# Optimization experiments

Hardware: AMD Instinct MI355X
Metric: run time of the kernel (lower is better)

## Reference

```python
import jax, jax.numpy as jnp
import numpy as np

B, T = 512, 2048
IN1, H1, H2 = 1, 64, 16


def _lstm_params(key, in_dim, hid):
    k = 1.0 / np.sqrt(hid)
    ks = jax.random.split(key, 4)
    u = lambda kk, shape: jax.random.uniform(kk, shape, jnp.float32, -k, k)
    return (u(ks[0], (4 * hid, in_dim)),  # w_ih, PyTorch gate order i,f,g,o
            u(ks[1], (4 * hid, hid)),     # w_hh
            u(ks[2], (4 * hid,)),         # b_ih
            u(ks[3], (4 * hid,)))         # b_hh


def setup_inputs() -> dict:
    key = jax.random.key(0)
    kx, k1, k2 = jax.random.split(key, 3)
    x = jax.random.normal(kx, (B, T, IN1), dtype=jnp.float32)
    w_ih1, w_hh1, b_ih1, b_hh1 = _lstm_params(k1, IN1, H1)
    w_ih2, w_hh2, b_ih2, b_hh2 = _lstm_params(k2, H1, H2)
    return {"x": x,
            "w_ih1": w_ih1, "w_hh1": w_hh1, "b_ih1": b_ih1, "b_hh1": b_hh1,
            "w_ih2": w_ih2, "w_hh2": w_hh2, "b_ih2": b_ih2, "b_hh2": b_hh2}


def _lstm(x, w_ih, w_hh, b_ih, b_hh):
    # x: [B, T, in]; returns all hidden states [B, T, H]
    hid = w_hh.shape[1]
    # precompute input contribution for every timestep: [T, B, 4H]
    xg = jnp.einsum('bti,gi->tbg', x, w_ih) + b_ih + b_hh
    h0 = jnp.zeros((x.shape[0], hid), x.dtype)
    c0 = jnp.zeros((x.shape[0], hid), x.dtype)

    def step(carry, xt):
        h, c = carry
        gates = xt + h @ w_hh.T                       # [B, 4H]
        i, f, g, o = jnp.split(gates, 4, axis=-1)     # PyTorch order
        i = jax.nn.sigmoid(i)
        f = jax.nn.sigmoid(f)
        g = jnp.tanh(g)
        o = jax.nn.sigmoid(o)
        c = f * c + i * g
        h = o * jnp.tanh(c)
        return (h, c), h

    _, hs = jax.lax.scan(step, (h0, c0), xg)          # hs: [T, B, H]
    return jnp.transpose(hs, (1, 0, 2))               # [B, T, H]


def reference(x, w_ih1, w_hh1, b_ih1, b_hh1, w_ih2, w_hh2, b_ih2, b_hh2):
    h1 = _lstm(x, w_ih1, w_hh1, b_ih1, b_hh1)   # [B, T, 64]
    h2 = _lstm(h1, w_ih2, w_hh2, b_ih2, b_hh2)  # [B, T, 16]
    return h2
```

## Files before the change

kernel.cpp:

```cpp
#include <hip/hip_runtime.h>

#define TSTEPS 2048
#define NBATCH 512
#define H1 64
#define H2 16

typedef _Float16 h2v __attribute__((ext_vector_type(2)));

__device__ __forceinline__ float fsig(float x) {
    return __builtin_amdgcn_rcpf(1.0f + __builtin_amdgcn_exp2f(-1.4426950408889634f * x));
}
__device__ __forceinline__ float ftanh(float x) {
    return 1.0f - 2.0f * __builtin_amdgcn_rcpf(1.0f + __builtin_amdgcn_exp2f(2.8853900817779268f * x));
}
__device__ __forceinline__ float act(float x, float k2) {
    return k2 * fsig(k2 * x) - (k2 - 1.0f);
}

#if __has_builtin(__builtin_amdgcn_fdot2)
__device__ __forceinline__ float dot2(int wp, int hp, float acc) {
    return __builtin_amdgcn_fdot2(__builtin_bit_cast(h2v, wp),
                                  __builtin_bit_cast(h2v, hp), acc, false);
}
#else
__device__ __forceinline__ float dot2(int wp, int hp, float acc) {
    h2v a = __builtin_bit_cast(h2v, wp), b = __builtin_bit_cast(h2v, hp);
    return acc + (float)a.x * (float)b.x + (float)a.y * (float)b.y;
}
#endif

__device__ __forceinline__ int packh2(float a, float b) {
    h2v v; v.x = (_Float16)a; v.y = (_Float16)b;
    return __builtin_bit_cast(int, v);
}
template<int CTRL>
__device__ __forceinline__ float dpp_bcast(float v) {
    int r = __builtin_amdgcn_mov_dpp(__float_as_int(v), CTRL, 0xF, 0xF, true);
    return __int_as_float(r);
}

__global__ void __launch_bounds__(64, 1)
__attribute__((amdgpu_waves_per_eu(1, 1)))
lstm2_fused(const float* __restrict__ x,
            const float* __restrict__ w_ih1,
            const float* __restrict__ w_hh1,
            const float* __restrict__ b_ih1,
            const float* __restrict__ b_hh1,
            const float* __restrict__ w_ih2,
            const float* __restrict__ w_hh2,
            const float* __restrict__ b_ih2,
            const float* __restrict__ b_hh2,
            float* __restrict__ out)
{
    const int lane = threadIdx.x;
    const int b    = blockIdx.x;

    __shared__ int4     wlds[26][64];
    __shared__ float    x_lds[TSTEPS];
    __shared__ _Float16 h1_lds[H1];
    __shared__ _Float16 h2_lds[H2];
    __shared__ float    ring[32][H2];

    {
        const float4* xs = (const float4*)(x + (size_t)b * TSTEPS);
        float4* xd = (float4*)x_lds;
        #pragma unroll
        for (int i = 0; i < 8; ++i) xd[lane + 64 * i] = xs[lane + 64 * i];
    }
    if (lane < 32) ((int*)h1_lds)[lane] = 0;
    if (lane < 8)  ((int*)h2_lds)[lane] = 0;

    int w1i[32], w1f[32];
    {
        const float* wri = w_hh1 + (size_t)lane * H1;
        const float* wrf = w_hh1 + (size_t)(H1 + lane) * H1;
        #pragma unroll
        for (int k = 0; k < 32; ++k) {
            w1i[k] = packh2(wri[2 * k], wri[2 * k + 1]);
            w1f[k] = packh2(wrf[2 * k], wrf[2 * k + 1]);
        }
    }
    const int m  = lane >> 2;
    const int g2 = lane & 3;
    const int r2 = g2 * H2 + m;
    {
        const float* wrg = w_hh1 + (size_t)(2 * H1 + lane) * H1;
        const float* wro = w_hh1 + (size_t)(3 * H1 + lane) * H1;
        const float* wr2 = w_ih2 + (size_t)r2 * H1;
        #pragma unroll
        for (int tq = 0; tq < 8; ++tq) {
            wlds[tq][lane] = make_int4(
                packh2(wrg[8*tq+0], wrg[8*tq+1]), packh2(wrg[8*tq+2], wrg[8*tq+3]),
                packh2(wrg[8*tq+4], wrg[8*tq+5]), packh2(wrg[8*tq+6], wrg[8*tq+7]));
            wlds[8 + tq][lane] = make_int4(
                packh2(wro[8*tq+0], wro[8*tq+1]), packh2(wro[8*tq+2], wro[8*tq+3]),
                packh2(wro[8*tq+4], wro[8*tq+5]), packh2(wro[8*tq+6], wro[8*tq+7]));
            wlds[16 + tq][lane] = make_int4(
                packh2(wr2[8*tq+0], wr2[8*tq+1]), packh2(wr2[8*tq+2], wr2[8*tq+3]),
                packh2(wr2[8*tq+4], wr2[8*tq+5]), packh2(wr2[8*tq+6], wr2[8*tq+7]));
        }
        const float* wrh = w_hh2 + (size_t)r2 * H2;
        wlds[24][lane] = make_int4(packh2(wrh[0], wrh[1]),  packh2(wrh[2], wrh[3]),
                                   packh2(wrh[4], wrh[5]),  packh2(wrh[6], wrh[7]));
        wlds[25][lane] = make_int4(packh2(wrh[8], wrh[9]),  packh2(wrh[10], wrh[11]),
                                   packh2(wrh[12], wrh[13]), packh2(wrh[14], wrh[15]));
    }

    const float wxi = w_ih1[lane],        wxf = w_ih1[H1 + lane];
    const float wxg = w_ih1[2*H1 + lane], wxo = w_ih1[3*H1 + lane];
    const float bsi = b_ih1[lane] + b_hh1[lane];
    const float bsf = b_ih1[H1+lane] + b_hh1[H1+lane];
    const float bsg = b_ih1[2*H1+lane] + b_hh1[2*H1+lane];
    const float bso = b_ih1[3*H1+lane] + b_hh1[3*H1+lane];
    const float bs2 = b_ih2[r2] + b_hh2[r2];
    const float k22 = (g2 == 2) ? 2.0f : 1.0f;

    float c1 = 0.0f;
    float c2 = 0.0f;
    float* outb = out + (size_t)b * TSTEPS * H2;

    const int4* wl = &wlds[0][0];

    for (int p = 0; p <= TSTEPS; ++p) {
        const int tau_f = p - 1;
        if (tau_f >= 31 && (tau_f & 15) == 15) {
            const int tau0 = (tau_f & ~15) - 16;
            const int tt = tau0 + (lane >> 2), ch0 = (lane & 3) * 4;
            float4 v = *(const float4*)&ring[tt & 31][ch0];
            *(float4*)(outb + (size_t)tt * H2 + ch0) = v;
        }

        const float xv = x_lds[p & (TSTEPS - 1)];
        float ai = bsi + wxi * xv;
        float af = bsf + wxf * xv;
        float ag = bsg + wxg * xv;
        float ao = bso + wxo * xv;
        float a0 = bs2, a1 = 0.f, a2a = 0.f, a3 = 0.f;
        int4 vh0, vh1;

        {
            const int4* hs4 = (const int4*)h1_lds;
            #pragma unroll
            for (int c = 0; c < 4; ++c) {
                int4 hA = hs4[2*c], hB = hs4[2*c + 1];
                int4 cg  = wl[(2*c)      * 64 + lane];
                int4 cg2 = wl[(2*c + 1)  * 64 + lane];
                int4 co  = wl[(8 + 2*c)  * 64 + lane];
                int4 co2 = wl[(9 + 2*c)  * 64 + lane];
                int4 cu  = wl[(16 + 2*c) * 64 + lane];
                int4 cu2 = wl[(17 + 2*c) * 64 + lane];
                if (c == 2) { vh0 = wl[24 * 64 + lane]; vh1 = wl[25 * 64 + lane]; }

                ai = dot2(w1i[8*c+0], hA.x, ai); ai = dot2(w1i[8*c+1], hA.y, ai);
                ai = dot2(w1i[8*c+2], hA.z, ai); ai = dot2(w1i[8*c+3], hA.w, ai);
                ai = dot2(w1i[8*c+4], hB.x, ai); ai = dot2(w1i[8*c+5], hB.y, ai);
                ai = dot2(w1i[8*c+6], hB.z, ai); ai = dot2(w1i[8*c+7], hB.w, ai);

                af = dot2(w1f[8*c+0], hA.x, af); af = dot2(w1f[8*c+1], hA.y, af);
                af = dot2(w1f[8*c+2], hA.z, af); af = dot2(w1f[8*c+3], hA.w, af);
                af = dot2(w1f[8*c+4], hB.x, af); af = dot2(w1f[8*c+5], hB.y, af);
                af = dot2(w1f[8*c+6], hB.z, af); af = dot2(w1f[8*c+7], hB.w, af);

                ag = dot2(cg.x,  hA.x, ag); ag = dot2(cg.y,  hA.y, ag);
                ag = dot2(cg.z,  hA.z, ag); ag = dot2(cg.w,  hA.w, ag);
                ag = dot2(cg2.x, hB.x, ag); ag = dot2(cg2.y, hB.y, ag);
                ag = dot2(cg2.z, hB.z, ag); ag = dot2(cg2.w, hB.w, ag);

                ao = dot2(co.x,  hA.x, ao); ao = dot2(co.y,  hA.y, ao);
                ao = dot2(co.z,  hA.z, ao); ao = dot2(co.w,  hA.w, ao);
                ao = dot2(co2.x, hB.x, ao); ao = dot2(co2.y, hB.y, ao);
                ao = dot2(co2.z, hB.z, ao); ao = dot2(co2.w, hB.w, ao);

                a0  = dot2(cu.x,  hA.x, a0);  a1  = dot2(cu.y,  hA.y, a1);
                a2a = dot2(cu.z,  hA.z, a2a); a3  = dot2(cu.w,  hA.w, a3);
                a0  = dot2(cu2.x, hB.x, a0);  a1  = dot2(cu2.y, hB.y, a1);
                a2a = dot2(cu2.z, hB.z, a2a); a3  = dot2(cu2.w, hB.w, a3);
            }
        }

        if (p < TSTEPS) {
            float gi = fsig(ai), gf = fsig(af), gg = ftanh(ag), go = fsig(ao);
            c1 = gf * c1 + gi * gg;
            float h1n = go * ftanh(c1);
            h1_lds[lane] = (_Float16)h1n;
        }

        if (p >= 1) {
            const int4* hs = (const int4*)h2_lds;
            int4 u0 = hs[0], u1 = hs[1];
            a0  = dot2(vh0.x, u0.x, a0);  a1  = dot2(vh0.y, u0.y, a1);
            a2a = dot2(vh0.z, u0.z, a2a); a3  = dot2(vh0.w, u0.w, a3);
            a0  = dot2(vh1.x, u1.x, a0);  a1  = dot2(vh1.y, u1.y, a1);
            a2a = dot2(vh1.z, u1.z, a2a); a3  = dot2(vh1.w, u1.w, a3);
            float av = act((a0 + a1) + (a2a + a3), k22);
            float gi = dpp_bcast<0x00>(av);
            float gf = dpp_bcast<0x55>(av);
            float gg = dpp_bcast<0xAA>(av);
            float go = dpp_bcast<0xFF>(av);
            c2 = gf * c2 + gi * gg;
            float h2n = go * ftanh(c2);
            if (g2 == 0) {
                h2_lds[m] = (_Float16)h2n;
                ring[(p - 1) & 31][m] = h2n;
            }
        }
    }

    {
        const int tt = 2032 + (lane >> 2), ch0 = (lane & 3) * 4;
        float4 v = *(const float4*)&ring[tt & 31][ch0];
        *(float4*)(outb + (size_t)tt * H2 + ch0) = v;
    }
}

extern "C" void kernel_launch(void* const* d_in, const int* in_sizes, int n_in,
                              void* d_out, int out_size, void* d_ws, size_t ws_size,
                              hipStream_t stream) {
    const float* x     = (const float*)d_in[0];
    const float* w_ih1 = (const float*)d_in[1];
    const float* w_hh1 = (const float*)d_in[2];
    const float* b_ih1 = (const float*)d_in[3];
    const float* b_hh1 = (const float*)d_in[4];
    const float* w_ih2 = (const float*)d_in[5];
    const float* w_hh2 = (const float*)d_in[6];
    const float* b_ih2 = (const float*)d_in[7];
    const float* b_hh2 = (const float*)d_in[8];
    float* out = (float*)d_out;

    lstm2_fused<<<NBATCH, 64, 0, stream>>>(x, w_ih1, w_hh1, b_ih1, b_hh1,
                                           w_ih2, w_hh2, b_ih2, b_hh2, out);
}
```

Baseline: 1.170 ms.

## Broadcast hidden states via readlane/DPP into SGPRs instead of LDS round-trip

Replaces the per-step LDS write/read of the layer-1 and layer-2 hidden vectors with cross-lane communication: each lane packs its fp16 hidden value with its neighbour's via a DPP xor-1 swap, and v_readlane broadcasts the packed pairs into uniform registers that feed the dot products directly. It also splits each gate accumulator into two partial sums to shorten the serial dependency chain. This removes LDS store-to-load latency and waitcnt stalls from the recurrent critical path, at the cost of 40 readlane instructions per step, which are serialising VALU-to-SGPR moves, plus added register pressure.

```diff
diff --git a/kernel.cpp b/kernel.cpp
--- a/kernel.cpp
+++ b/kernel.cpp
@@ -37,6 +37,9 @@
 __device__ __forceinline__ float dpp_bcast(float v) {
     int r = __builtin_amdgcn_mov_dpp(__float_as_int(v), CTRL, 0xF, 0xF, true);
     return __int_as_float(r);
+}
+__device__ __forceinline__ int dpp_xor1_i(int v) {
+    return __builtin_amdgcn_mov_dpp(v, 0xB1, 0xF, 0xF, true);
 }
 
 __global__ void __launch_bounds__(64, 1)
@@ -55,11 +58,9 @@
     const int lane = threadIdx.x;
     const int b    = blockIdx.x;
 
-    __shared__ int4     wlds[26][64];
-    __shared__ float    x_lds[TSTEPS];
-    __shared__ _Float16 h1_lds[H1];
-    __shared__ _Float16 h2_lds[H2];
-    __shared__ float    ring[32][H2];
+    __shared__ int4  wlds[26][64];
+    __shared__ float x_lds[TSTEPS];
+    __shared__ float ring[32][H2];
 
     {
         const float4* xs = (const float4*)(x + (size_t)b * TSTEPS);
@@ -67,8 +68,6 @@
         #pragma unroll
         for (int i = 0; i < 8; ++i) xd[lane + 64 * i] = xs[lane + 64 * i];
     }
-    if (lane < 32) ((int*)h1_lds)[lane] = 0;
-    if (lane < 8)  ((int*)h2_lds)[lane] = 0;
 
     int w1i[32], w1f[32];
     {
@@ -121,6 +120,13 @@
 
     const int4* wl = &wlds[0][0];
 
+    int sh[32];
+    int s2h[8];
+    #pragma unroll
+    for (int i = 0; i < 32; ++i) sh[i] = 0;
+    #pragma unroll
+    for (int i = 0; i < 8; ++i)  s2h[i] = 0;
+
     for (int p = 0; p <= TSTEPS; ++p) {
         const int tau_f = p - 1;
         if (tau_f >= 31 && (tau_f & 15) == 15) {
@@ -131,67 +137,72 @@
         }
 
         const float xv = x_lds[p & (TSTEPS - 1)];
-        float ai = bsi + wxi * xv;
-        float af = bsf + wxf * xv;
-        float ag = bsg + wxg * xv;
-        float ao = bso + wxo * xv;
+        float aiA = bsi + wxi * xv, aiB = 0.f;
+        float afA = bsf + wxf * xv, afB = 0.f;
+        float agA = bsg + wxg * xv, agB = 0.f;
+        float aoA = bso + wxo * xv, aoB = 0.f;
         float a0 = bs2, a1 = 0.f, a2a = 0.f, a3 = 0.f;
         int4 vh0, vh1;
 
-        {
-            const int4* hs4 = (const int4*)h1_lds;
-            #pragma unroll
-            for (int c = 0; c < 4; ++c) {
-                int4 hA = hs4[2*c], hB = hs4[2*c + 1];
-                int4 cg  = wl[(2*c)      * 64 + lane];
-                int4 cg2 = wl[(2*c + 1)  * 64 + lane];
-                int4 co  = wl[(8 + 2*c)  * 64 + lane];
-                int4 co2 = wl[(9 + 2*c)  * 64 + lane];
-                int4 cu  = wl[(16 + 2*c) * 64 + lane];
-                int4 cu2 = wl[(17 + 2*c) * 64 + lane];
-                if (c == 2) { vh0 = wl[24 * 64 + lane]; vh1 = wl[25 * 64 + lane]; }
-
-                ai = dot2(w1i[8*c+0], hA.x, ai); ai = dot2(w1i[8*c+1], hA.y, ai);
-                ai = dot2(w1i[8*c+2], hA.z, ai); ai = dot2(w1i[8*c+3], hA.w, ai);
-                ai = dot2(w1i[8*c+4], hB.x, ai); ai = dot2(w1i[8*c+5], hB.y, ai);
-                ai = dot2(w1i[8*c+6], hB.z, ai); ai = dot2(w1i[8*c+7], hB.w, ai);
-
-                af = dot2(w1f[8*c+0], hA.x, af); af = dot2(w1f[8*c+1], hA.y, af);
-                af = dot2(w1f[8*c+2], hA.z, af); af = dot2(w1f[8*c+3], hA.w, af);
-                af = dot2(w1f[8*c+4], hB.x, af); af = dot2(w1f[8*c+5], hB.y, af);
-                af = dot2(w1f[8*c+6], hB.z, af); af = dot2(w1f[8*c+7], hB.w, af);
-
-                ag = dot2(cg.x,  hA.x, ag); ag = dot2(cg.y,  hA.y, ag);
-                ag = dot2(cg.z,  hA.z, ag); ag = dot2(cg.w,  hA.w, ag);
-                ag = dot2(cg2.x, hB.x, ag); ag = dot2(cg2.y, hB.y, ag);
-                ag = dot2(cg2.z, hB.z, ag); ag = dot2(cg2.w, hB.w, ag);
-
-                ao = dot2(co.x,  hA.x, ao); ao = dot2(co.y,  hA.y, ao);
-                ao = dot2(co.z,  hA.z, ao); ao = dot2(co.w,  hA.w, ao);
-                ao = dot2(co2.x, hB.x, ao); ao = dot2(co2.y, hB.y, ao);
-                ao = dot2(co2.z, hB.z, ao); ao = dot2(co2.w, hB.w, ao);
-
-                a0  = dot2(cu.x,  hA.x, a0);  a1  = dot2(cu.y,  hA.y, a1);
-                a2a = dot2(cu.z,  hA.z, a2a); a3  = dot2(cu.w,  hA.w, a3);
-                a0  = dot2(cu2.x, hB.x, a0);  a1  = dot2(cu2.y, hB.y, a1);
-                a2a = dot2(cu2.z, hB.z, a2a); a3  = dot2(cu2.w, hB.w, a3);
-            }
+        #pragma unroll
+        for (int c = 0; c < 4; ++c) {
+            int4 cg  = wl[(2*c)      * 64 + lane];
+            int4 cg2 = wl[(2*c + 1)  * 64 + lane];
+            int4 co  = wl[(8 + 2*c)  * 64 + lane];
+            int4 co2 = wl[(9 + 2*c)  * 64 + lane];
+            int4 cu  = wl[(16 + 2*c) * 64 + lane];
+            int4 cu2 = wl[(17 + 2*c) * 64 + lane];
+            if (c == 2) { vh0 = wl[24 * 64 + lane]; vh1 = wl[25 * 64 + lane]; }
+            float* pi = (c < 2) ? &aiA : &aiB;
+            float* pf = (c < 2) ? &afA : &afB;
+            float* pg = (c < 2) ? &agA : &agB;
+            float* po = (c < 2) ? &aoA : &aoB;
+
+            *pi = dot2(w1i[8*c+0], sh[8*c+0], *pi); *pi = dot2(w1i[8*c+1], sh[8*c+1], *pi);
+            *pi = dot2(w1i[8*c+2], sh[8*c+2], *pi); *pi = dot2(w1i[8*c+3], sh[8*c+3], *pi);
+            *pi = dot2(w1i[8*c+4], sh[8*c+4], *pi); *pi = dot2(w1i[8*c+5], sh[8*c+5], *pi);
+            *pi = dot2(w1i[8*c+6], sh[8*c+6], *pi); *pi = dot2(w1i[8*c+7], sh[8*c+7], *pi);
+
+            *pf = dot2(w1f[8*c+0], sh[8*c+0], *pf); *pf = dot2(w1f[8*c+1], sh[8*c+1], *pf);
+            *pf = dot2(w1f[8*c+2], sh[8*c+2], *pf); *pf = dot2(w1f[8*c+3], sh[8*c+3], *pf);
+            *pf = dot2(w1f[8*c+4], sh[8*c+4], *pf); *pf = dot2(w1f[8*c+5], sh[8*c+5], *pf);
+            *pf = dot2(w1f[8*c+6], sh[8*c+6], *pf); *pf = dot2(w1f[8*c+7], sh[8*c+7], *pf);
+
+            *pg = dot2(cg.x,  sh[8*c+0], *pg); *pg = dot2(cg.y,  sh[8*c+1], *pg);
+            *pg = dot2(cg.z,  sh[8*c+2], *pg); *pg = dot2(cg.w,  sh[8*c+3], *pg);
+            *pg = dot2(cg2.x, sh[8*c+4], *pg); *pg = dot2(cg2.y, sh[8*c+5], *pg);
+            *pg = dot2(cg2.z, sh[8*c+6], *pg); *pg = dot2(cg2.w, sh[8*c+7], *pg);
+
+            *po = dot2(co.x,  sh[8*c+0], *po); *po = dot2(co.y,  sh[8*c+1], *po);
+            *po = dot2(co.z,  sh[8*c+2], *po); *po = dot2(co.w,  sh[8*c+3], *po);
+            *po = dot2(co2.x, sh[8*c+4], *po); *po = dot2(co2.y, sh[8*c+5], *po);
+            *po = dot2(co2.z, sh[8*c+6], *po); *po = dot2(co2.w, sh[8*c+7], *po);
+
+            a0  = dot2(cu.x,  sh[8*c+0], a0);  a1  = dot2(cu.y,  sh[8*c+1], a1);
+            a2a = dot2(cu.z,  sh[8*c+2], a2a); a3  = dot2(cu.w,  sh[8*c+3], a3);
+            a0  = dot2(cu2.x, sh[8*c+4], a0);  a1  = dot2(cu2.y, sh[8*c+5], a1);
+            a2a = dot2(cu2.z, sh[8*c+6], a2a); a3  = dot2(cu2.w, sh[8*c+7], a3);
         }
 
         if (p < TSTEPS) {
-            float gi = fsig(ai), gf = fsig(af), gg = ftanh(ag), go = fsig(ao);
+            float gi = fsig(aiA + aiB), gf = fsig(afA + afB);
+            float gg = ftanh(agA + agB), go = fsig(aoA + aoB);
             c1 = gf * c1 + gi * gg;
             float h1n = go * ftanh(c1);
-            h1_lds[lane] = (_Float16)h1n;
+            h2v hv; hv.x = (_Float16)h1n; hv.y = (_Float16)0.0f;
+            int h1u = __builtin_bit_cast(int, hv) & 0xFFFF;
+            int nb  = dpp_xor1_i(h1u);
+            int packed = h1u | (nb << 16);
+            #pragma unroll
+            for (int i = 0; i < 32; ++i)
+                sh[i] = __builtin_amdgcn_readlane(packed, 2 * i);
         }
 
         if (p >= 1) {
-            const int4* hs = (const int4*)h2_lds;
-            int4 u0 = hs[0], u1 = hs[1];
-            a0  = dot2(vh0.x, u0.x, a0);  a1  = dot2(vh0.y, u0.y, a1);
-            a2a = dot2(vh0.z, u0.z, a2a); a3  = dot2(vh0.w, u0.w, a3);
-            a0  = dot2(vh1.x, u1.x, a0);  a1  = dot2(vh1.y, u1.y, a1);
-            a2a = dot2(vh1.z, u1.z, a2a); a3  = dot2(vh1.w, u1.w, a3);
+            a0  = dot2(vh0.x, s2h[0], a0);  a1  = dot2(vh0.y, s2h[1], a1);
+            a2a = dot2(vh0.z, s2h[2], a2a); a3  = dot2(vh0.w, s2h[3], a3);
+            a0  = dot2(vh1.x, s2h[4], a0);  a1  = dot2(vh1.y, s2h[5], a1);
+            a2a = dot2(vh1.z, s2h[6], a2a); a3  = dot2(vh1.w, s2h[7], a3);
             float av = act((a0 + a1) + (a2a + a3), k22);
             float gi = dpp_bcast<0x00>(av);
             float gf = dpp_bcast<0x55>(av);
@@ -199,10 +210,15 @@
             float go = dpp_bcast<0xFF>(av);
             c2 = gf * c2 + gi * gg;
             float h2n = go * ftanh(c2);
-            if (g2 == 0) {
-                h2_lds[m] = (_Float16)h2n;
-                ring[(p - 1) & 31][m] = h2n;
+            h2v h2p; h2p.x = (_Float16)h2n; h2p.y = (_Float16)0.0f;
+            int h2u = __builtin_bit_cast(int, h2p) & 0xFFFF;
+            #pragma unroll
+            for (int k = 0; k < 8; ++k) {
+                int lo = __builtin_amdgcn_readlane(h2u, 8 * k);
+                int hi = __builtin_amdgcn_readlane(h2u, 8 * k + 4);
+                s2h[k] = lo | (hi << 16);
             }
+            if (g2 == 0) ring[(p - 1) & 31][m] = h2n;
         }
     }
 
```

Result: slower. 1.299 ms (+11.0%).

## Process two batch rows per wavefront to interleave independent recurrences

Applied to the files above, without the earlier changes.

Each 64-lane block now runs two batch sequences at once, so each weight load from LDS or registers is reused for two independent dot-product chains. The forget-gate weights move from registers to LDS to make room for the doubled accumulators and states. The intent is to hide the serial latency of the per-step recurrence with a second independent chain and to reuse weight loads across two rows. The grid halves to 256 blocks, so fewer wavefronts run across the CUs, and each step now does twice the work.

```diff
diff --git a/kernel.cpp b/kernel.cpp
--- a/kernel.cpp
+++ b/kernel.cpp
@@ -53,56 +53,58 @@
             float* __restrict__ out)
 {
     const int lane = threadIdx.x;
-    const int b    = blockIdx.x;
-
-    __shared__ int4     wlds[26][64];
-    __shared__ float    x_lds[TSTEPS];
-    __shared__ _Float16 h1_lds[H1];
-    __shared__ _Float16 h2_lds[H2];
-    __shared__ float    ring[32][H2];
-
-    {
-        const float4* xs = (const float4*)(x + (size_t)b * TSTEPS);
-        float4* xd = (float4*)x_lds;
+    const int b0   = blockIdx.x * 2;
+
+    __shared__ int4     wlds[34][64];
+    __shared__ float    x_lds[2][TSTEPS];
+    __shared__ _Float16 h1_lds[2][H1];
+    __shared__ _Float16 h2_lds[2][H2];
+    __shared__ float    ring[32][2][H2];
+
+    #pragma unroll
+    for (int bb = 0; bb < 2; ++bb) {
+        const float4* xs = (const float4*)(x + (size_t)(b0 + bb) * TSTEPS);
+        float4* xd = (float4*)x_lds[bb];
         #pragma unroll
         for (int i = 0; i < 8; ++i) xd[lane + 64 * i] = xs[lane + 64 * i];
     }
-    if (lane < 32) ((int*)h1_lds)[lane] = 0;
-    if (lane < 8)  ((int*)h2_lds)[lane] = 0;
-
-    int w1i[32], w1f[32];
+    h1_lds[0][lane] = (_Float16)0.0f;
+    h1_lds[1][lane] = (_Float16)0.0f;
+    if (lane < 16) { h2_lds[0][lane] = (_Float16)0.0f; h2_lds[1][lane] = (_Float16)0.0f; }
+
+    int w1i[32];
     {
         const float* wri = w_hh1 + (size_t)lane * H1;
-        const float* wrf = w_hh1 + (size_t)(H1 + lane) * H1;
-        #pragma unroll
-        for (int k = 0; k < 32; ++k) {
-            w1i[k] = packh2(wri[2 * k], wri[2 * k + 1]);
-            w1f[k] = packh2(wrf[2 * k], wrf[2 * k + 1]);
-        }
+        #pragma unroll
+        for (int k = 0; k < 32; ++k) w1i[k] = packh2(wri[2 * k], wri[2 * k + 1]);
     }
     const int m  = lane >> 2;
     const int g2 = lane & 3;
     const int r2 = g2 * H2 + m;
     {
+        const float* wrf = w_hh1 + (size_t)(H1 + lane) * H1;
         const float* wrg = w_hh1 + (size_t)(2 * H1 + lane) * H1;
         const float* wro = w_hh1 + (size_t)(3 * H1 + lane) * H1;
         const float* wr2 = w_ih2 + (size_t)r2 * H1;
         #pragma unroll
-        for (int tq = 0; tq < 8; ++tq) {
-            wlds[tq][lane] = make_int4(
-                packh2(wrg[8*tq+0], wrg[8*tq+1]), packh2(wrg[8*tq+2], wrg[8*tq+3]),
-                packh2(wrg[8*tq+4], wrg[8*tq+5]), packh2(wrg[8*tq+6], wrg[8*tq+7]));
-            wlds[8 + tq][lane] = make_int4(
-                packh2(wro[8*tq+0], wro[8*tq+1]), packh2(wro[8*tq+2], wro[8*tq+3]),
-                packh2(wro[8*tq+4], wro[8*tq+5]), packh2(wro[8*tq+6], wro[8*tq+7]));
-            wlds[16 + tq][lane] = make_int4(
-                packh2(wr2[8*tq+0], wr2[8*tq+1]), packh2(wr2[8*tq+2], wr2[8*tq+3]),
-                packh2(wr2[8*tq+4], wr2[8*tq+5]), packh2(wr2[8*tq+6], wr2[8*tq+7]));
+        for (int r = 0; r < 8; ++r) {
+            wlds[r][lane] = make_int4(
+                packh2(wrf[8*r+0], wrf[8*r+1]), packh2(wrf[8*r+2], wrf[8*r+3]),
+                packh2(wrf[8*r+4], wrf[8*r+5]), packh2(wrf[8*r+6], wrf[8*r+7]));
+            wlds[8 + r][lane] = make_int4(
+                packh2(wrg[8*r+0], wrg[8*r+1]), packh2(wrg[8*r+2], wrg[8*r+3]),
+                packh2(wrg[8*r+4], wrg[8*r+5]), packh2(wrg[8*r+6], wrg[8*r+7]));
+            wlds[16 + r][lane] = make_int4(
+                packh2(wro[8*r+0], wro[8*r+1]), packh2(wro[8*r+2], wro[8*r+3]),
+                packh2(wro[8*r+4], wro[8*r+5]), packh2(wro[8*r+6], wro[8*r+7]));
+            wlds[24 + r][lane] = make_int4(
+                packh2(wr2[8*r+0], wr2[8*r+1]), packh2(wr2[8*r+2], wr2[8*r+3]),
+                packh2(wr2[8*r+4], wr2[8*r+5]), packh2(wr2[8*r+6], wr2[8*r+7]));
         }
         const float* wrh = w_hh2 + (size_t)r2 * H2;
-        wlds[24][lane] = make_int4(packh2(wrh[0], wrh[1]),  packh2(wrh[2], wrh[3]),
+        wlds[32][lane] = make_int4(packh2(wrh[0], wrh[1]),  packh2(wrh[2], wrh[3]),
                                    packh2(wrh[4], wrh[5]),  packh2(wrh[6], wrh[7]));
-        wlds[25][lane] = make_int4(packh2(wrh[8], wrh[9]),  packh2(wrh[10], wrh[11]),
+        wlds[33][lane] = make_int4(packh2(wrh[8], wrh[9]),  packh2(wrh[10], wrh[11]),
                                    packh2(wrh[12], wrh[13]), packh2(wrh[14], wrh[15]));
     }
 
@@ -115,101 +117,128 @@
     const float bs2 = b_ih2[r2] + b_hh2[r2];
     const float k22 = (g2 == 2) ? 2.0f : 1.0f;
 
-    float c1 = 0.0f;
-    float c2 = 0.0f;
-    float* outb = out + (size_t)b * TSTEPS * H2;
+    float c1_0 = 0.f, c1_1 = 0.f;
+    float c2_0 = 0.f, c2_1 = 0.f;
+    float* outb0 = out + (size_t)b0 * TSTEPS * H2;
+    float* outb1 = out + (size_t)(b0 + 1) * TSTEPS * H2;
 
     const int4* wl = &wlds[0][0];
+
+#define DOTS1(C, hA, hB, ai, af, ag, ao, q0, q1, q2, q3) do {                  \
+    ai = dot2(w1i[8*C+0], hA.x, ai); ai = dot2(w1i[8*C+1], hA.y, ai);          \
+    ai = dot2(w1i[8*C+2], hA.z, ai); ai = dot2(w1i[8*C+3], hA.w, ai);          \
+    ai = dot2(w1i[8*C+4], hB.x, ai); ai = dot2(w1i[8*C+5], hB.y, ai);          \
+    ai = dot2(w1i[8*C+6], hB.z, ai); ai = dot2(w1i[8*C+7], hB.w, ai);          \
+    af = dot2(cf.x,  hA.x, af); af = dot2(cf.y,  hA.y, af);                    \
+    af = dot2(cf.z,  hA.z, af); af = dot2(cf.w,  hA.w, af);                    \
+    af = dot2(cf2.x, hB.x, af); af = dot2(cf2.y, hB.y, af);                    \
+    af = dot2(cf2.z, hB.z, af); af = dot2(cf2.w, hB.w, af);                    \
+    ag = dot2(cg.x,  hA.x, ag); ag = dot2(cg.y,  hA.y, ag);                    \
+    ag = dot2(cg.z,  hA.z, ag); ag = dot2(cg.w,  hA.w, ag);                    \
+    ag = dot2(cg2.x, hB.x, ag); ag = dot2(cg2.y, hB.y, ag);                    \
+    ag = dot2(cg2.z, hB.z, ag); ag = dot2(cg2.w, hB.w, ag);                    \
+    ao = dot2(co.x,  hA.x, ao); ao = dot2(co.y,  hA.y, ao);                    \
+    ao = dot2(co.z,  hA.z, ao); ao = dot2(co.w,  hA.w, ao);                    \
+    ao = dot2(co2.x, hB.x, ao); ao = dot2(co2.y, hB.y, ao);                    \
+    ao = dot2(co2.z, hB.z, ao); ao = dot2(co2.w, hB.w, ao);                    \
+    q0 = dot2(cu.x,  hA.x, q0); q1 = dot2(cu.y,  hA.y, q1);                    \
+    q2 = dot2(cu.z,  hA.z, q2); q3 = dot2(cu.w,  hA.w, q3);                    \
+    q0 = dot2(cu2.x, hB.x, q0); q1 = dot2(cu2.y, hB.y, q1);                    \
+    q2 = dot2(cu2.z, hB.z, q2); q3 = dot2(cu2.w, hB.w, q3);                    \
+} while (0)
 
     for (int p = 0; p <= TSTEPS; ++p) {
         const int tau_f = p - 1;
         if (tau_f >= 31 && (tau_f & 15) == 15) {
             const int tau0 = (tau_f & ~15) - 16;
             const int tt = tau0 + (lane >> 2), ch0 = (lane & 3) * 4;
-            float4 v = *(const float4*)&ring[tt & 31][ch0];
-            *(float4*)(outb + (size_t)tt * H2 + ch0) = v;
-        }
-
-        const float xv = x_lds[p & (TSTEPS - 1)];
-        float ai = bsi + wxi * xv;
-        float af = bsf + wxf * xv;
-        float ag = bsg + wxg * xv;
-        float ao = bso + wxo * xv;
-        float a0 = bs2, a1 = 0.f, a2a = 0.f, a3 = 0.f;
+            float4 v0 = *(const float4*)&ring[tt & 31][0][ch0];
+            float4 v1 = *(const float4*)&ring[tt & 31][1][ch0];
+            *(float4*)(outb0 + (size_t)tt * H2 + ch0) = v0;
+            *(float4*)(outb1 + (size_t)tt * H2 + ch0) = v1;
+        }
+
+        const int pm = p & (TSTEPS - 1);
+        const float xv0 = x_lds[0][pm], xv1 = x_lds[1][pm];
+        float ai0 = bsi + wxi * xv0, af0 = bsf + wxf * xv0;
+        float ag0 = bsg + wxg * xv0, ao0 = bso + wxo * xv0;
+        float ai1 = bsi + wxi * xv1, af1 = bsf + wxf * xv1;
+        float ag1 = bsg + wxg * xv1, ao1 = bso + wxo * xv1;
+        float q00 = bs2, q10 = 0.f, q20 = 0.f, q30 = 0.f;
+        float q01 = bs2, q11 = 0.f, q21 = 0.f, q31 = 0.f;
         int4 vh0, vh1;
 
-        {
-            const int4* hs4 = (const int4*)h1_lds;
-            #pragma unroll
-            for (int c = 0; c < 4; ++c) {
-                int4 hA = hs4[2*c], hB = hs4[2*c + 1];
-                int4 cg  = wl[(2*c)      * 64 + lane];
-                int4 cg2 = wl[(2*c + 1)  * 64 + lane];
-                int4 co  = wl[(8 + 2*c)  * 64 + lane];
-                int4 co2 = wl[(9 + 2*c)  * 64 + lane];
-                int4 cu  = wl[(16 + 2*c) * 64 + lane];
-                int4 cu2 = wl[(17 + 2*c) * 64 + lane];
-                if (c == 2) { vh0 = wl[24 * 64 + lane]; vh1 = wl[25 * 64 + lane]; }
-
-                ai = dot2(w1i[8*c+0], hA.x, ai); ai = dot2(w1i[8*c+1], hA.y, ai);
-                ai = dot2(w1i[8*c+2], hA.z, ai); ai = dot2(w1i[8*c+3], hA.w, ai);
-                ai = dot2(w1i[8*c+4], hB.x, ai); ai = dot2(w1i[8*c+5], hB.y, ai);
-                ai = dot2(w1i[8*c+6], hB.z, ai); ai = dot2(w1i[8*c+7], hB.w, ai);
-
-                af = dot2(w1f[8*c+0], hA.x, af); af = dot2(w1f[8*c+1], hA.y, af);
-                af = dot2(w1f[8*c+2], hA.z, af); af = dot2(w1f[8*c+3], hA.w, af);
-                af = dot2(w1f[8*c+4], hB.x, af); af = dot2(w1f[8*c+5], hB.y, af);
-                af = dot2(w1f[8*c+6], hB.z, af); af = dot2(w1f[8*c+7], hB.w, af);
-
-                ag = dot2(cg.x,  hA.x, ag); ag = dot2(cg.y,  hA.y, ag);
-                ag = dot2(cg.z,  hA.z, ag); ag = dot2(cg.w,  hA.w, ag);
-                ag = dot2(cg2.x, hB.x, ag); ag = dot2(cg2.y, hB.y, ag);
-                ag = dot2(cg2.z, hB.z, ag); ag = dot2(cg2.w, hB.w, ag);
-
-                ao = dot2(co.x,  hA.x, ao); ao = dot2(co.y,  hA.y, ao);
-                ao = dot2(co.z,  hA.z, ao); ao = dot2(co.w,  hA.w, ao);
-                ao = dot2(co2.x, hB.x, ao); ao = dot2(co2.y, hB.y, ao);
-                ao = dot2(co2.z, hB.z, ao); ao = dot2(co2.w, hB.w, ao);
-
-                a0  = dot2(cu.x,  hA.x, a0);  a1  = dot2(cu.y,  hA.y, a1);
-                a2a = dot2(cu.z,  hA.z, a2a); a3  = dot2(cu.w,  hA.w, a3);
-                a0  = dot2(cu2.x, hB.x, a0);  a1  = dot2(cu2.y, hB.y, a1);
-                a2a = dot2(cu2.z, hB.z, a2a); a3  = dot2(cu2.w, hB.w, a3);
+        const int4* hs0 = (const int4*)h1_lds[0];
+        const int4* hs1 = (const int4*)h1_lds[1];
+
+        #pragma unroll
+        for (int c = 0; c < 4; ++c) {
+            int4 cf  = wl[(2*c)      * 64 + lane];
+            int4 cf2 = wl[(2*c + 1)  * 64 + lane];
+            int4 cg  = wl[(8 + 2*c)  * 64 + lane];
+            int4 cg2 = wl[(9 + 2*c)  * 64 + lane];
+            int4 co  = wl[(16 + 2*c) * 64 + lane];
+            int4 co2 = wl[(17 + 2*c) * 64 + lane];
+            int4 cu  = wl[(24 + 2*c) * 64 + lane];
+            int4 cu2 = wl[(25 + 2*c) * 64 + lane];
+            if (c == 2) { vh0 = wl[32 * 64 + lane]; vh1 = wl[33 * 64 + lane]; }
+            int4 hA0 = hs0[2*c], hB0 = hs0[2*c + 1];
+            int4 hA1 = hs1[2*c], hB1 = hs1[2*c + 1];
+            DOTS1(c, hA0, hB0, ai0, af0, ag0, ao0, q00, q10, q20, q30);
+            DOTS1(c, hA1, hB1, ai1, af1, ag1, ao1, q01, q11, q21, q31);
+        }
+
+        if (p < TSTEPS) {
+            float gi0 = fsig(ai0), gf0 = fsig(af0), gg0 = ftanh(ag0), go0 = fsig(ao0);
+            float gi1 = fsig(ai1), gf1 = fsig(af1), gg1 = ftanh(ag1), go1 = fsig(ao1);
+            c1_0 = gf0 * c1_0 + gi0 * gg0;
+            c1_1 = gf1 * c1_1 + gi1 * gg1;
+            float h1n0 = go0 * ftanh(c1_0);
+            float h1n1 = go1 * ftanh(c1_1);
+            h1_lds[0][lane] = (_Float16)h1n0;
+            h1_lds[1][lane] = (_Float16)h1n1;
+        }
+
+        if (p >= 1) {
+            const int4* h2p0 = (const int4*)h2_lds[0];
+            const int4* h2p1 = (const int4*)h2_lds[1];
+            int4 u00 = h2p0[0], u01 = h2p0[1];
+            int4 u10 = h2p1[0], u11 = h2p1[1];
+            q00 = dot2(vh0.x, u00.x, q00); q10 = dot2(vh0.y, u00.y, q10);
+            q20 = dot2(vh0.z, u00.z, q20); q30 = dot2(vh0.w, u00.w, q30);
+            q00 = dot2(vh1.x, u01.x, q00); q10 = dot2(vh1.y, u01.y, q10);
+            q20 = dot2(vh1.z, u01.z, q20); q30 = dot2(vh1.w, u01.w, q30);
+            q01 = dot2(vh0.x, u10.x, q01); q11 = dot2(vh0.y, u10.y, q11);
+            q21 = dot2(vh0.z, u10.z, q21); q31 = dot2(vh0.w, u10.w, q31);
+            q01 = dot2(vh1.x, u11.x, q01); q11 = dot2(vh1.y, u11.y, q11);
+            q21 = dot2(vh1.z, u11.z, q21); q31 = dot2(vh1.w, u11.w, q31);
+
+            float av0 = act((q00 + q10) + (q20 + q30), k22);
+            float av1 = act((q01 + q11) + (q21 + q31), k22);
+            float gi0 = dpp_bcast<0x00>(av0), gf0 = dpp_bcast<0x55>(av0);
+            float gg0 = dpp_bcast<0xAA>(av0), go0 = dpp_bcast<0xFF>(av0);
+            float gi1 = dpp_bcast<0x00>(av1), gf1 = dpp_bcast<0x55>(av1);
+            float gg1 = dpp_bcast<0xAA>(av1), go1 = dpp_bcast<0xFF>(av1);
+            c2_0 = gf0 * c2_0 + gi0 * gg0;
+            c2_1 = gf1 * c2_1 + gi1 * gg1;
+            float h2n0 = go0 * ftanh(c2_0);
+            float h2n1 = go1 * ftanh(c2_1);
+            if (g2 == 0) {
+                h2_lds[0][m] = (_Float16)h2n0;
+                h2_lds[1][m] = (_Float16)h2n1;
+                ring[(p - 1) & 31][0][m] = h2n0;
+                ring[(p - 1) & 31][1][m] = h2n1;
             }
         }
-
-        if (p < TSTEPS) {
-            float gi = fsig(ai), gf = fsig(af), gg = ftanh(ag), go = fsig(ao);
-            c1 = gf * c1 + gi * gg;
-            float h1n = go * ftanh(c1);
-            h1_lds[lane] = (_Float16)h1n;
-        }
-
-        if (p >= 1) {
-            const int4* hs = (const int4*)h2_lds;
-            int4 u0 = hs[0], u1 = hs[1];
-            a0  = dot2(vh0.x, u0.x, a0);  a1  = dot2(vh0.y, u0.y, a1);
-            a2a = dot2(vh0.z, u0.z, a2a); a3  = dot2(vh0.w, u0.w, a3);
-            a0  = dot2(vh1.x, u1.x, a0);  a1  = dot2(vh1.y, u1.y, a1);
-            a2a = dot2(vh1.z, u1.z, a2a); a3  = dot2(vh1.w, u1.w, a3);
-            float av = act((a0 + a1) + (a2a + a3), k22);
-            float gi = dpp_bcast<0x00>(av);
-            float gf = dpp_bcast<0x55>(av);
-            float gg = dpp_bcast<0xAA>(av);
-            float go = dpp_bcast<0xFF>(av);
-            c2 = gf * c2 + gi * gg;
-            float h2n = go * ftanh(c2);
-            if (g2 == 0) {
-                h2_lds[m] = (_Float16)h2n;
-                ring[(p - 1) & 31][m] = h2n;
-            }
-        }
-    }
+    }
+#undef DOTS1
 
     {
         const int tt = 2032 + (lane >> 2), ch0 = (lane & 3) * 4;
-        float4 v = *(const float4*)&ring[tt & 31][ch0];
-        *(float4*)(outb + (size_t)tt * H2 + ch0) = v;
+        float4 v0 = *(const float4*)&ring[tt & 31][0][ch0];
+        float4 v1 = *(const float4*)&ring[tt & 31][1][ch0];
+        *(float4*)(outb0 + (size_t)tt * H2 + ch0) = v0;
+        *(float4*)(outb1 + (size_t)tt * H2 + ch0) = v1;
     }
 }
 
@@ -227,6 +256,6 @@
     const float* b_hh2 = (const float*)d_in[8];
     float* out = (float*)d_out;
 
-    lstm2_fused<<<NBATCH, 64, 0, stream>>>(x, w_ih1, w_hh1, b_ih1, b_hh1,
-                                           w_ih2, w_hh2, b_ih2, b_hh2, out);
-}
+    lstm2_fused<<<NBATCH / 2, 64, 0, stream>>>(x, w_ih1, w_hh1, b_ih1, b_hh1,
+                                               w_ih2, w_hh2, b_ih2, b_hh2, out);
+}
```

Measured after the change: 2.184 ms. +86.7%, slower.

## Split LSTM layers into producer/consumer wavefronts with LDS ring handoff

Applied to the files above, without the earlier changes.

Launches 128 threads per block so one wave runs layer 1 and a second wave runs layer 2. They hand off h1 through a 64-entry LDS ring, with volatile progress counters and s_sleep spin-waits for flow control. This takes the layer-2 input projection off the layer-1 critical path, and layer-2 weights now live in registers instead of LDS. In exchange it adds spin-wait synchronisation, relies only on compiler barriers and volatile accesses for memory ordering, and replaces the batched ring-buffer output stores with per-step scalar global stores.

```diff
diff --git a/kernel.cpp b/kernel.cpp
--- a/kernel.cpp
+++ b/kernel.cpp
@@ -39,7 +39,7 @@
     return __int_as_float(r);
 }
 
-__global__ void __launch_bounds__(64, 1)
+__global__ void __launch_bounds__(128, 1)
 __attribute__((amdgpu_waves_per_eu(1, 1)))
 lstm2_fused(const float* __restrict__ x,
             const float* __restrict__ w_ih1,
@@ -52,26 +52,30 @@
             const float* __restrict__ b_hh2,
             float* __restrict__ out)
 {
-    const int lane = threadIdx.x;
+    const int tid  = threadIdx.x;
+    const int lane = tid & 63;
     const int b    = blockIdx.x;
 
-    __shared__ int4     wlds[26][64];
+    __shared__ int4     wgo[16][64];
     __shared__ float    x_lds[TSTEPS];
-    __shared__ _Float16 h1_lds[H1];
-    __shared__ _Float16 h2_lds[H2];
-    __shared__ float    ring[32][H2];
-
-    {
+    __shared__ _Float16 h1ring[64][H1];
+    __shared__ _Float16 h2buf[H2];
+    __shared__ int      prog_s;
+    __shared__ int      cons_s;
+
+    volatile int* vprog = &prog_s;
+    volatile int* vcons = &cons_s;
+
+    int   w1i[32], w1f[32];
+    float wxi = 0, wxf = 0, wxg = 0, wxo = 0, bsi = 0, bsf = 0, bsg = 0, bso = 0;
+    int   w2r[32], wh2r[8];
+    float bs2 = 0, k22 = 1.f;
+
+    if (tid < 64) {
         const float4* xs = (const float4*)(x + (size_t)b * TSTEPS);
         float4* xd = (float4*)x_lds;
         #pragma unroll
         for (int i = 0; i < 8; ++i) xd[lane + 64 * i] = xs[lane + 64 * i];
-    }
-    if (lane < 32) ((int*)h1_lds)[lane] = 0;
-    if (lane < 8)  ((int*)h2_lds)[lane] = 0;
-
-    int w1i[32], w1f[32];
-    {
         const float* wri = w_hh1 + (size_t)lane * H1;
         const float* wrf = w_hh1 + (size_t)(H1 + lane) * H1;
         #pragma unroll
@@ -79,137 +83,140 @@
             w1i[k] = packh2(wri[2 * k], wri[2 * k + 1]);
             w1f[k] = packh2(wrf[2 * k], wrf[2 * k + 1]);
         }
-    }
-    const int m  = lane >> 2;
-    const int g2 = lane & 3;
-    const int r2 = g2 * H2 + m;
-    {
         const float* wrg = w_hh1 + (size_t)(2 * H1 + lane) * H1;
         const float* wro = w_hh1 + (size_t)(3 * H1 + lane) * H1;
-        const float* wr2 = w_ih2 + (size_t)r2 * H1;
-        #pragma unroll
-        for (int tq = 0; tq < 8; ++tq) {
-            wlds[tq][lane] = make_int4(
-                packh2(wrg[8*tq+0], wrg[8*tq+1]), packh2(wrg[8*tq+2], wrg[8*tq+3]),
-                packh2(wrg[8*tq+4], wrg[8*tq+5]), packh2(wrg[8*tq+6], wrg[8*tq+7]));
-            wlds[8 + tq][lane] = make_int4(
-                packh2(wro[8*tq+0], wro[8*tq+1]), packh2(wro[8*tq+2], wro[8*tq+3]),
-                packh2(wro[8*tq+4], wro[8*tq+5]), packh2(wro[8*tq+6], wro[8*tq+7]));
-            wlds[16 + tq][lane] = make_int4(
-                packh2(wr2[8*tq+0], wr2[8*tq+1]), packh2(wr2[8*tq+2], wr2[8*tq+3]),
-                packh2(wr2[8*tq+4], wr2[8*tq+5]), packh2(wr2[8*tq+6], wr2[8*tq+7]));
-        }
-        const float* wrh = w_hh2 + (size_t)r2 * H2;
-        wlds[24][lane] = make_int4(packh2(wrh[0], wrh[1]),  packh2(wrh[2], wrh[3]),
-                                   packh2(wrh[4], wrh[5]),  packh2(wrh[6], wrh[7]));
-        wlds[25][lane] = make_int4(packh2(wrh[8], wrh[9]),  packh2(wrh[10], wrh[11]),
-                                   packh2(wrh[12], wrh[13]), packh2(wrh[14], wrh[15]));
+        #pragma unroll
+        for (int r = 0; r < 8; ++r) {
+            wgo[r][lane] = make_int4(
+                packh2(wrg[8*r+0], wrg[8*r+1]), packh2(wrg[8*r+2], wrg[8*r+3]),
+                packh2(wrg[8*r+4], wrg[8*r+5]), packh2(wrg[8*r+6], wrg[8*r+7]));
+            wgo[8 + r][lane] = make_int4(
+                packh2(wro[8*r+0], wro[8*r+1]), packh2(wro[8*r+2], wro[8*r+3]),
+                packh2(wro[8*r+4], wro[8*r+5]), packh2(wro[8*r+6], wro[8*r+7]));
+        }
+        wxi = w_ih1[lane];          wxf = w_ih1[H1 + lane];
+        wxg = w_ih1[2*H1 + lane];   wxo = w_ih1[3*H1 + lane];
+        bsi = b_ih1[lane]        + b_hh1[lane];
+        bsf = b_ih1[H1 + lane]   + b_hh1[H1 + lane];
+        bsg = b_ih1[2*H1 + lane] + b_hh1[2*H1 + lane];
+        bso = b_ih1[3*H1 + lane] + b_hh1[3*H1 + lane];
+        if (lane == 0) *vprog = 0;
+    } else {
+        const int m = lane >> 2, g2 = lane & 3;
+        const int r2 = g2 * H2 + m;
+        #pragma unroll
+        for (int k = 0; k < 32; ++k)
+            w2r[k] = packh2(w_ih2[(size_t)r2 * H1 + 2*k], w_ih2[(size_t)r2 * H1 + 2*k + 1]);
+        #pragma unroll
+        for (int k = 0; k < 8; ++k)
+            wh2r[k] = packh2(w_hh2[(size_t)r2 * H2 + 2*k], w_hh2[(size_t)r2 * H2 + 2*k + 1]);
+        bs2 = b_ih2[r2] + b_hh2[r2];
+        k22 = (g2 == 2) ? 2.0f : 1.0f;
+        if (lane < 16) h2buf[lane] = (_Float16)0.0f;
+        if (lane == 0) *vcons = 0;
     }
-
-    const float wxi = w_ih1[lane],        wxf = w_ih1[H1 + lane];
-    const float wxg = w_ih1[2*H1 + lane], wxo = w_ih1[3*H1 + lane];
-    const float bsi = b_ih1[lane] + b_hh1[lane];
-    const float bsf = b_ih1[H1+lane] + b_hh1[H1+lane];
-    const float bsg = b_ih1[2*H1+lane] + b_hh1[2*H1+lane];
-    const float bso = b_ih1[3*H1+lane] + b_hh1[3*H1+lane];
-    const float bs2 = b_ih2[r2] + b_hh2[r2];
-    const float k22 = (g2 == 2) ? 2.0f : 1.0f;
-
-    float c1 = 0.0f;
-    float c2 = 0.0f;
-    float* outb = out + (size_t)b * TSTEPS * H2;
-
-    const int4* wl = &wlds[0][0];
-
-    for (int p = 0; p <= TSTEPS; ++p) {
-        const int tau_f = p - 1;
-        if (tau_f >= 31 && (tau_f & 15) == 15) {
-            const int tau0 = (tau_f & ~15) - 16;
-            const int tt = tau0 + (lane >> 2), ch0 = (lane & 3) * 4;
-            float4 v = *(const float4*)&ring[tt & 31][ch0];
-            *(float4*)(outb + (size_t)tt * H2 + ch0) = v;
-        }
-
-        const float xv = x_lds[p & (TSTEPS - 1)];
-        float ai = bsi + wxi * xv;
-        float af = bsf + wxf * xv;
-        float ag = bsg + wxg * xv;
-        float ao = bso + wxo * xv;
-        float a0 = bs2, a1 = 0.f, a2a = 0.f, a3 = 0.f;
-        int4 vh0, vh1;
-
-        {
-            const int4* hs4 = (const int4*)h1_lds;
+    __syncthreads();
+
+    if (tid < 64) {
+        float c1 = 0.0f;
+        int4 hp[8];
+        #pragma unroll
+        for (int i = 0; i < 8; ++i) hp[i] = make_int4(0, 0, 0, 0);
+
+        for (int t = 0; t < TSTEPS; ++t) {
+            if (t >= 64 && (t & 31) == 0) {
+                while (*vcons < t - 32) __builtin_amdgcn_s_sleep(8);
+            }
+            const float xv = x_lds[t];
+            float ai = bsi + wxi * xv, af = bsf + wxf * xv;
+            float ag = bsg + wxg * xv, ao = bso + wxo * xv;
             #pragma unroll
             for (int c = 0; c < 4; ++c) {
-                int4 hA = hs4[2*c], hB = hs4[2*c + 1];
-                int4 cg  = wl[(2*c)      * 64 + lane];
-                int4 cg2 = wl[(2*c + 1)  * 64 + lane];
-                int4 co  = wl[(8 + 2*c)  * 64 + lane];
-                int4 co2 = wl[(9 + 2*c)  * 64 + lane];
-                int4 cu  = wl[(16 + 2*c) * 64 + lane];
-                int4 cu2 = wl[(17 + 2*c) * 64 + lane];
-                if (c == 2) { vh0 = wl[24 * 64 + lane]; vh1 = wl[25 * 64 + lane]; }
-
+                int4 cg  = wgo[2*c][lane],     cg2 = wgo[2*c + 1][lane];
+                int4 co  = wgo[8 + 2*c][lane], co2 = wgo[9 + 2*c][lane];
+                int4 hA = hp[2*c], hB = hp[2*c + 1];
                 ai = dot2(w1i[8*c+0], hA.x, ai); ai = dot2(w1i[8*c+1], hA.y, ai);
                 ai = dot2(w1i[8*c+2], hA.z, ai); ai = dot2(w1i[8*c+3], hA.w, ai);
                 ai = dot2(w1i[8*c+4], hB.x, ai); ai = dot2(w1i[8*c+5], hB.y, ai);
                 ai = dot2(w1i[8*c+6], hB.z, ai); ai = dot2(w1i[8*c+7], hB.w, ai);
-
                 af = dot2(w1f[8*c+0], hA.x, af); af = dot2(w1f[8*c+1], hA.y, af);
                 af = dot2(w1f[8*c+2], hA.z, af); af = dot2(w1f[8*c+3], hA.w, af);
                 af = dot2(w1f[8*c+4], hB.x, af); af = dot2(w1f[8*c+5], hB.y, af);
                 af = dot2(w1f[8*c+6], hB.z, af); af = dot2(w1f[8*c+7], hB.w, af);
-
                 ag = dot2(cg.x,  hA.x, ag); ag = dot2(cg.y,  hA.y, ag);
                 ag = dot2(cg.z,  hA.z, ag); ag = dot2(cg.w,  hA.w, ag);
                 ag = dot2(cg2.x, hB.x, ag); ag = dot2(cg2.y, hB.y, ag);
                 ag = dot2(cg2.z, hB.z, ag); ag = dot2(cg2.w, hB.w, ag);
-
                 ao = dot2(co.x,  hA.x, ao); ao = dot2(co.y,  hA.y, ao);
                 ao = dot2(co.z,  hA.z, ao); ao = dot2(co.w,  hA.w, ao);
                 ao = dot2(co2.x, hB.x, ao); ao = dot2(co2.y, hB.y, ao);
                 ao = dot2(co2.z, hB.z, ao); ao = dot2(co2.w, hB.w, ao);
-
-                a0  = dot2(cu.x,  hA.x, a0);  a1  = dot2(cu.y,  hA.y, a1);
-                a2a = dot2(cu.z,  hA.z, a2a); a3  = dot2(cu.w,  hA.w, a3);
-                a0  = dot2(cu2.x, hB.x, a0);  a1  = dot2(cu2.y, hB.y, a1);
-                a2a = dot2(cu2.z, hB.z, a2a); a3  = dot2(cu2.w, hB.w, a3);
-            }
-        }
-
-        if (p < TSTEPS) {
+            }
             float gi = fsig(ai), gf = fsig(af), gg = ftanh(ag), go = fsig(ao);
             c1 = gf * c1 + gi * gg;
             float h1n = go * ftanh(c1);
-            h1_lds[lane] = (_Float16)h1n;
-        }
-
-        if (p >= 1) {
-            const int4* hs = (const int4*)h2_lds;
-            int4 u0 = hs[0], u1 = hs[1];
-            a0  = dot2(vh0.x, u0.x, a0);  a1  = dot2(vh0.y, u0.y, a1);
-            a2a = dot2(vh0.z, u0.z, a2a); a3  = dot2(vh0.w, u0.w, a3);
-            a0  = dot2(vh1.x, u1.x, a0);  a1  = dot2(vh1.y, u1.y, a1);
-            a2a = dot2(vh1.z, u1.z, a2a); a3  = dot2(vh1.w, u1.w, a3);
-            float av = act((a0 + a1) + (a2a + a3), k22);
-            float gi = dpp_bcast<0x00>(av);
-            float gf = dpp_bcast<0x55>(av);
-            float gg = dpp_bcast<0xAA>(av);
-            float go = dpp_bcast<0xFF>(av);
+            h1ring[t & 63][lane] = (_Float16)h1n;
+            asm volatile("" ::: "memory");
+            if (lane == 0) *vprog = t + 1;
+            asm volatile("" ::: "memory");
+            const int4* hs = (const int4*)h1ring[t & 63];
+            #pragma unroll
+            for (int i = 0; i < 8; ++i) hp[i] = hs[i];
+        }
+    } else {
+        const int m = lane >> 2, g2 = lane & 3;
+        float c2 = 0.0f;
+        int seen = 0;
+        float* outb = out + (size_t)b * TSTEPS * H2;
+
+        for (int t = 0; t < TSTEPS; ++t) {
+            if (seen < t + 1) {
+                while ((seen = *vprog) < t + 1) __builtin_amdgcn_s_sleep(8);
+            }
+            asm volatile("" ::: "memory");
+            const int4* hs = (const int4*)h1ring[t & 63];
+            int4 hA = hs[0], hB = hs[1], hC = hs[2], hD = hs[3];
+            int4 hE = hs[4], hF = hs[5], hG = hs[6], hH = hs[7];
+
+            float q0 = bs2, q1 = 0.f, q2 = 0.f, q3 = 0.f;
+            q0 = dot2(w2r[0],  hA.x, q0); q1 = dot2(w2r[1],  hA.y, q1);
+            q2 = dot2(w2r[2],  hA.z, q2); q3 = dot2(w2r[3],  hA.w, q3);
+            q0 = dot2(w2r[4],  hB.x, q0); q1 = dot2(w2r[5],  hB.y, q1);
+            q2 = dot2(w2r[6],  hB.z, q2); q3 = dot2(w2r[7],  hB.w, q3);
+            q0 = dot2(w2r[8],  hC.x, q0); q1 = dot2(w2r[9],  hC.y, q1);
+            q2 = dot2(w2r[10], hC.z, q2); q3 = dot2(w2r[11], hC.w, q3);
+            q0 = dot2(w2r[12], hD.x, q0); q1 = dot2(w2r[13], hD.y, q1);
+            q2 = dot2(w2r[14], hD.z, q2); q3 = dot2(w2r[15], hD.w, q3);
+            q0 = dot2(w2r[16], hE.x, q0); q1 = dot2(w2r[17], hE.y, q1);
+            q2 = dot2(w2r[18], hE.z, q2); q3 = dot2(w2r[19], hE.w, q3);
+            q0 = dot2(w2r[20], hF.x, q0); q1 = dot2(w2r[21], hF.y, q1);
+            q2 = dot2(w2r[22], hF.z, q2); q3 = dot2(w2r[23], hF.w, q3);
+            q0 = dot2(w2r[24], hG.x, q0); q1 = dot2(w2r[25], hG.y, q1);
+            q2 = dot2(w2r[26], hG.z, q2); q3 = dot2(w2r[27], hG.w, q3);
+            q0 = dot2(w2r[28], hH.x, q0); q1 = dot2(w2r[29], hH.y, q1);
+            q2 = dot2(w2r[30], hH.z, q2); q3 = dot2(w2r[31], hH.w, q3);
+
+            const int4* h2p = (const int4*)h2buf;
+            int4 u0 = h2p[0], u1 = h2p[1];
+            q0 = dot2(wh2r[0], u0.x, q0); q1 = dot2(wh2r[1], u0.y, q1);
+            q2 = dot2(wh2r[2], u0.z, q2); q3 = dot2(wh2r[3], u0.w, q3);
+            q0 = dot2(wh2r[4], u1.x, q0); q1 = dot2(wh2r[5], u1.y, q1);
+            q2 = dot2(wh2r[6], u1.z, q2); q3 = dot2(wh2r[7], u1.w, q3);
+
+            float av = act((q0 + q1) + (q2 + q3), k22);
+            float gi = dpp_bcast<0x00>(av), gf = dpp_bcast<0x55>(av);
+            float gg = dpp_bcast<0xAA>(av), go = dpp_bcast<0xFF>(av);
             c2 = gf * c2 + gi * gg;
             float h2n = go * ftanh(c2);
             if (g2 == 0) {
-                h2_lds[m] = (_Float16)h2n;
-                ring[(p - 1) & 31][m] = h2n;
-            }
-        }
-    }
-
-    {
-        const int tt = 2032 + (lane >> 2), ch0 = (lane & 3) * 4;
-        float4 v = *(const float4*)&ring[tt & 31][ch0];
-        *(float4*)(outb + (size_t)tt * H2 + ch0) = v;
+                h2buf[m] = (_Float16)h2n;
+                outb[(size_t)t * H2 + m] = h2n;
+            }
+            if ((t & 15) == 15) {
+                asm volatile("" ::: "memory");
+                if (lane == 0) *vcons = t + 1;
+            }
+        }
     }
 }
 
@@ -227,6 +234,6 @@
     const float* b_hh2 = (const float*)d_in[8];
     float* out = (float*)d_out;
 
-    lstm2_fused<<<NBATCH, 64, 0, stream>>>(x, w_ih1, w_hh1, b_ih1, b_hh1,
-                                           w_ih2, w_hh2, b_ih2, b_hh2, out);
-}
+    lstm2_fused<<<NBATCH, 128, 0, stream>>>(x, w_ih1, w_hh1, b_ih1, b_hh1,
+                                            w_ih2, w_hh2, b_ih2, b_hh2, out);
+}
```

New measurement: 1.306 ms. +11.6%, slower.
